# Performance work log

Measured on AMD Instinct MI355X. Metric: run time of the kernel, lower is better.

## Reference

```python
import jax, jax.numpy as jnp
from jax import lax
import numpy as np

K = 4            # prototypes per class: 3 kmeans centroids + 1 backbone
EPS = 0.1        # sinkhorn entropic regularization
MAX_ITER = 100
THRESH = 0.01
KM_ITERS = 10    # Lloyd iterations (replaces host-side sklearn KMeans)
HW = 28          # the original reshapes pred to 28x28, fixing n = 784


def setup_inputs():
    key = jax.random.key(0)
    k1, k2, k3, k4 = jax.random.split(key, 4)
    b, n, d, c = 32, HW * HW, 1024, 20
    return {
        "query": jax.random.normal(k1, (b, n, d), dtype=jnp.float32),
        "score": jax.random.uniform(k2, (b, n, c), dtype=jnp.float32),
        "label": jax.random.randint(k3, (b, c), 0, 2),
        "gt": jax.random.randint(k4, (b, HW, HW), 0, c + 1),
        "weights": jnp.array([1.0, 1.0, 0.0, -1.0], dtype=jnp.float32),
    }


def _assign(dq, cen, selfm):
    # dq [b,m,d], cen [b,c,j,d], selfm [b,c,m] float mask -> one-hot labels, counts
    x2 = jnp.sum(dq * dq, axis=-1)                                   # [b,m]
    d2 = (x2[:, None, :, None]
          - 2.0 * jnp.einsum('bmd,bcjd->bcmj', dq, cen)
          + jnp.sum(cen * cen, axis=-1)[:, :, None, :])              # [b,c,m,j]
    oh = jax.nn.one_hot(jnp.argmin(d2, axis=-1), cen.shape[2], dtype=dq.dtype) * selfm[..., None]
    return oh, oh.sum(axis=2)


def _sinkhorn(Km, u, v):
    # vectorized over the [b,c] pair grid, per-pair early exit as in the torch loop
    def cond(st):
        it, r, cc, done = st
        return (it < MAX_ITER) & jnp.logical_not(jnp.all(done))

    def body(st):
        it, r, cc, done = st
        r1 = u / jnp.einsum('bcnj,bcj->bcn', Km, cc)
        c1 = v / jnp.einsum('bcnj,bcn->bcj', Km, r1)
        err = jnp.mean(jnp.abs(r1 - r), axis=-1)                     # [b,c]
        r = jnp.where(done[..., None], r, r1)
        cc = jnp.where(done[..., None], cc, c1)
        done = done | (err < THRESH)
        return it + 1, r, cc, done

    st = (jnp.int32(0), jnp.ones_like(u), jnp.ones_like(v),
          jnp.zeros(Km.shape[:2], dtype=bool))
    _, r, cc, _ = lax.while_loop(cond, body, st)
    return r[..., :, None] * cc[..., None, :] * Km                   # [b,c,n,K]


def _forward(query, score, label, gt, weights):
    b, n, d = query.shape
    c = score.shape[2]
    dq, ds = query[:, ::2, :], score[:, ::2, :]                      # stride-2 downsample
    m = dq.shape[1]
    cls_assign = jnp.argmax(ds, axis=-1)                             # [b,m]
    sel = cls_assign[:, None, :] == jnp.arange(c)[None, :, None]     # [b,c,m]
    selfm = sel.astype(query.dtype)
    cnt = selfm.sum(-1)                                              # [b,c]
    valid = (label > 0) & (cnt >= K)

    # ---- masked Lloyd's k-means with k-1 = 3 clusters per (image, class) pair
    order = jnp.argsort((~sel).astype(jnp.int32), axis=-1)           # masked points first
    init_idx = order[..., :K - 1]                                    # [b,c,3]
    cen = dq[jnp.arange(b)[:, None, None], init_idx]                 # [b,c,3,d]

    def km_step(cen, _):
        oh, kcnt = _assign(dq, cen, selfm)
        sums = jnp.einsum('bmd,bcmj->bcjd', dq, oh)
        cen = jnp.where(kcnt[..., None] > 0,
                        sums / jnp.maximum(kcnt, 1.0)[..., None], cen)
        return cen, None

    cen, _ = lax.scan(km_step, cen, None, length=KM_ITERS)
    oh, kcnt = _assign(dq, cen, selfm)                               # final labels

    # ---- sort centroids by mean cluster score (descending)
    sm = ds.mean(axis=-1)                                            # [b,m]
    avg = jnp.where(kcnt > 0,
                    jnp.einsum('bm,bcmj->bcj', sm, oh) / jnp.maximum(kcnt, 1.0),
                    -jnp.inf)
    ordj = jnp.argsort(-avg, axis=-1)                                # [b,c,3]
    cen = jnp.take_along_axis(cen, ordj[..., None], axis=2)

    # ---- backbone prototype = mean over unselected downsampled tokens
    un = 1.0 - selfm
    backbone = jnp.einsum('bmd,bcm->bcd', dq, un) / jnp.maximum(m - cnt, 1.0)[..., None]
    protos = jnp.concatenate([cen, backbone[:, :, None, :]], axis=2)  # [b,c,4,d]

    # ---- OT between query[0] tokens and the 4 prototypes (original uses query[0] always)
    q0 = query[0]
    q0h = q0 / jnp.maximum(jnp.linalg.norm(q0, axis=-1, keepdims=True), 1e-12)
    ph = protos / jnp.maximum(jnp.linalg.norm(protos, axis=-1, keepdims=True), 1e-12)
    sim = jnp.einsum('nd,bcjd->bcnj', q0h, ph)                       # [b,c,n,4]
    Km = lax.stop_gradient(jnp.exp(-(1.0 - sim) / EPS))              # torch.no_grad
    u = jnp.full((b, c, n), 1.0 / n, dtype=query.dtype)
    v = jnp.full((b, c, K), 1.0 / K, dtype=query.dtype)
    T = lax.stop_gradient(_sinkhorn(Km, u, v))                       # [b,c,n,4]

    valid = valid & jnp.logical_not(jnp.any(jnp.isnan(T), axis=(2, 3)))
    pred = jnp.einsum('bcnj,j->bcn', T, weights)                     # [b,c,n]

    # ---- BCE vs gt masks (28x28 -> 28x28 bilinear resize is the identity)
    y = (gt.reshape(b, -1)[:, None, :] == (jnp.arange(c) + 1)[None, :, None]).astype(pred.dtype)
    p = jnp.clip(pred, 0.0, 1.0)
    bce = -(y * jnp.maximum(jnp.log(p), -100.0)
            + (1.0 - y) * jnp.maximum(jnp.log(1.0 - p), -100.0)).mean(axis=-1)  # [b,c]
    bce = jnp.where(valid, bce, 0.0)
    total_n = valid.sum().astype(pred.dtype)
    return bce.sum() / (total_n + 1e-4)


def reference(query, score, label, gt, weights):
    return _forward(query, score, label, gt, weights)
```

## Files before the change

kernel.cpp:

```cpp
#include <hip/hip_runtime.h>
#include <cmath>

#define BB 32
#define NN 784
#define MM 392
#define DD 1024
#define CC 20
#define JJ 3
#define KP 4
#define KM_ITERS 10
#define GMAX 64
#define SKK 3

__global__ void k_cls(const float* __restrict__ score, int* __restrict__ cls,
                      float* __restrict__ sm, int* __restrict__ cnt) {
  int t = blockIdx.x * blockDim.x + threadIdx.x;
  if (t >= BB * MM) return;
  int b = t / MM, i = t - b * MM;
  const float* s = score + ((size_t)b * NN + 2 * i) * CC;
  float best = s[0]; int bi = 0; float acc = s[0];
  #pragma unroll
  for (int c = 1; c < CC; c++) { float v = s[c]; acc += v; if (v > best) { best = v; bi = c; } }
  cls[t] = bi;
  sm[t] = acc / (float)CC;
  atomicAdd(&cnt[b * CC + bi], 1);
}

__global__ void k_valid(const int* __restrict__ label, const int* __restrict__ cnt,
                        int* __restrict__ vlist, int* __restrict__ cpos, int* __restrict__ nvp) {
  __shared__ int sf[1024];
  int t = threadIdx.x;
  int flag = 0;
  if (t < BB * CC) flag = (label[t] > 0 && cnt[t] >= KP) ? 1 : 0;
  sf[t] = flag;
  __syncthreads();
  for (int off = 1; off < 1024; off <<= 1) {
    int v = sf[t];
    int add = (t >= off) ? sf[t - off] : 0;
    __syncthreads();
    sf[t] = v + add;
    __syncthreads();
  }
  if (t < BB * CC) {
    int pos = sf[t] - flag;
    cpos[t] = flag ? pos : -1;
    if (flag) vlist[pos] = t;
  }
  if (t == 0) *nvp = sf[BB * CC - 1];
}

__global__ __launch_bounds__(512) void k_gram(
    const float* __restrict__ query, const int* __restrict__ cls,
    const int* __restrict__ cpos, const float* __restrict__ sm,
    float* __restrict__ classsum, float* __restrict__ ph) {
  int bc = blockIdx.x; int b = bc / CC, c = bc - b * CC;
  int tid = threadIdx.x, lane = tid & 63, wv = tid >> 6;
  const float* qb = query + (size_t)b * NN * DD;
  __shared__ int s_scan[512];
  __shared__ int s_list[GMAX];
  __shared__ __align__(16) float Xs[GMAX][68];
  __shared__ float Gl[GMAX][65];
  __shared__ float s_w[JJ][GMAX];
  __shared__ int s_rank[JJ];

  int flag = 0;
  if (tid < MM) flag = (cls[b * MM + tid] == c) ? 1 : 0;
  s_scan[tid] = flag;
  __syncthreads();
  for (int off = 1; off < 512; off <<= 1) {
    int v = s_scan[tid];
    int add = (tid >= off) ? s_scan[tid - off] : 0;
    __syncthreads();
    s_scan[tid] = v + add;
    __syncthreads();
  }
  if (tid < MM && flag) { int pp = s_scan[tid] - 1; if (pp < GMAX) s_list[pp] = tid; }
  __syncthreads();
  int mc = s_scan[MM - 1]; if (mc > GMAX) mc = GMAX;
  bool valid = (cpos[bc] >= 0);

  const float* pbase0 = nullptr; const float* pbase1 = nullptr;
  float* xdst0 = nullptr; float* xdst1 = nullptr;
  {
    int e0 = tid;
    if (e0 < mc * 16) {
      pbase0 = qb + (size_t)(2 * s_list[e0 >> 4]) * DD + (e0 & 15) * 4;
      xdst0 = &Xs[e0 >> 4][(e0 & 15) * 4];
    }
    int e1 = tid + 512;
    if (e1 < mc * 16) {
      pbase1 = qb + (size_t)(2 * s_list[e1 >> 4]) * DD + (e1 & 15) * 4;
      xdst1 = &Xs[e1 >> 4][(e1 & 15) * 4];
    }
  }

  int npairs = mc * (mc + 1) / 2;
  int pi[5], pj[5];
  float pacc[5];
  #pragma unroll
  for (int s = 0; s < 5; s++) {
    pacc[s] = 0.f; pi[s] = -1; pj[s] = 0;
    int p = tid + s * 512;
    if (valid && p < npairs) {
      int i = (int)floorf((sqrtf(8.0f * (float)p + 1.0f) - 1.0f) * 0.5f);
      while ((i + 1) * (i + 2) / 2 <= p) i++;
      while (i * (i + 1) / 2 > p) i--;
      pi[s] = i; pj[s] = p - i * (i + 1) / 2;
    }
  }

  float4 cur0, cur1, nxt0, nxt1;
  if (pbase0) cur0 = *(const float4*)(pbase0);
  if (pbase1) cur1 = *(const float4*)(pbase1);
  for (int ch = 0; ch < 16; ch++) {
    __syncthreads();
    if (pbase0) *(float4*)xdst0 = cur0;
    if (pbase1) *(float4*)xdst1 = cur1;
    if (ch < 15) {
      if (pbase0) nxt0 = *(const float4*)(pbase0 + (ch + 1) * 64);
      if (pbase1) nxt1 = *(const float4*)(pbase1 + (ch + 1) * 64);
    }
    __syncthreads();
    #pragma unroll
    for (int s = 0; s < 5; s++) {
      if (pi[s] >= 0) {
        const float4* xi = (const float4*)&Xs[pi[s]][0];
        const float4* xj = (const float4*)&Xs[pj[s]][0];
        float a = 0.f;
        #pragma unroll
        for (int kk = 0; kk < 16; kk++) {
          float4 u = xi[kk], w = xj[kk];
          a += u.x * w.x + u.y * w.y + u.z * w.z + u.w * w.w;
        }
        pacc[s] += a;
      }
    }
    if (tid >= 448) {
      int col = tid - 448;
      float ssum = 0.f;
      for (int row = 0; row < mc; row++) ssum += Xs[row][col];
      classsum[(size_t)bc * DD + ch * 64 + col] = ssum;
    }
    cur0 = nxt0; cur1 = nxt1;
  }
  if (!valid) return;

  #pragma unroll
  for (int s = 0; s < 5; s++)
    if (pi[s] >= 0) { Gl[pi[s]][pj[s]] = pacc[s]; Gl[pj[s]][pi[s]] = pacc[s]; }
  __syncthreads();

  if (wv == 0) {
    bool act = lane < mc;
    float smv = act ? sm[b * MM + s_list[lane]] : 0.f;
    s_w[0][lane] = (lane == 0) ? 1.f : 0.f;
    s_w[1][lane] = (lane == 1) ? 1.f : 0.f;
    s_w[2][lane] = (lane == 2) ? 1.f : 0.f;
    int aj = 0, n0 = 0, n1 = 0, n2 = 0;
    for (int it = 0; it <= KM_ITERS; it++) {
      float h0 = 0.f, h1 = 0.f, h2 = 0.f;
      if (act) {
        for (int i = 0; i < mc; i++) {
          float g = Gl[lane][i];
          h0 += s_w[0][i] * g; h1 += s_w[1][i] * g; h2 += s_w[2][i] * g;
        }
      }
      float t0 = s_w[0][lane] * h0, t1 = s_w[1][lane] * h1, t2 = s_w[2][lane] * h2;
      for (int o = 1; o < 64; o <<= 1) {
        t0 += __shfl_xor(t0, o, 64); t1 += __shfl_xor(t1, o, 64); t2 += __shfl_xor(t2, o, 64);
      }
      float e0 = t0 - 2.f * h0, e1 = t1 - 2.f * h1, e2 = t2 - 2.f * h2;
      aj = 0; float bv = e0;
      if (e1 < bv) { bv = e1; aj = 1; }
      if (e2 < bv) { bv = e2; aj = 2; }
      n0 = __popcll(__ballot(act && aj == 0));
      n1 = __popcll(__ballot(act && aj == 1));
      n2 = __popcll(__ballot(act && aj == 2));
      if (it == KM_ITERS) break;
      if (act) {
        if (n0 > 0) s_w[0][lane] = (aj == 0) ? 1.f / (float)n0 : 0.f;
        if (n1 > 0) s_w[1][lane] = (aj == 1) ? 1.f / (float)n1 : 0.f;
        if (n2 > 0) s_w[2][lane] = (aj == 2) ? 1.f / (float)n2 : 0.f;
      }
    }
    float s0 = (act && aj == 0) ? smv : 0.f;
    float s1 = (act && aj == 1) ? smv : 0.f;
    float s2 = (act && aj == 2) ? smv : 0.f;
    for (int o = 1; o < 64; o <<= 1) {
      s0 += __shfl_xor(s0, o, 64); s1 += __shfl_xor(s1, o, 64); s2 += __shfl_xor(s2, o, 64);
    }
    if (lane == 0) {
      float avg[JJ];
      avg[0] = (n0 > 0) ? s0 / (float)n0 : -INFINITY;
      avg[1] = (n1 > 0) ? s1 / (float)n1 : -INFINITY;
      avg[2] = (n2 > 0) ? s2 / (float)n2 : -INFINITY;
      bool used[JJ] = {false, false, false};
      for (int s = 0; s < JJ; s++) {
        int bi = -1; float bv = 0.f;
        for (int j = 0; j < JJ; j++)
          if (!used[j] && (bi < 0 || avg[j] > bv)) { bi = j; bv = avg[j]; }
        used[bi] = true; s_rank[bi] = s;
      }
    }
  }
  __syncthreads();

  float cenv[16];
  if (pbase0) cur0 = *(const float4*)(pbase0);
  if (pbase1) cur1 = *(const float4*)(pbase1);
  for (int ch = 0; ch < 16; ch++) {
    __syncthreads();
    if (pbase0) *(float4*)xdst0 = cur0;
    if (pbase1) *(float4*)xdst1 = cur1;
    if (ch < 15) {
      if (pbase0) nxt0 = *(const float4*)(pbase0 + (ch + 1) * 64);
      if (pbase1) nxt1 = *(const float4*)(pbase1 + (ch + 1) * 64);
    }
    __syncthreads();
    if (tid < 192) {
      int j = tid >> 6, l = tid & 63;
      float a = 0.f;
      for (int g = 0; g < mc; g++) a += s_w[j][g] * Xs[g][l];
      cenv[ch] = a;
    }
    cur0 = nxt0; cur1 = nxt1;
  }
  if (tid < 192) {
    int j = tid >> 6, l = tid & 63;
    float ssq = 0.f;
    #pragma unroll
    for (int ch = 0; ch < 16; ch++) ssq += cenv[ch] * cenv[ch];
    for (int o = 1; o < 64; o <<= 1) ssq += __shfl_xor(ssq, o, 64);
    float nrm = fmaxf(sqrtf(ssq), 1e-12f);
    float* dst = ph + ((size_t)bc * KP + s_rank[j]) * DD + l;
    #pragma unroll
    for (int ch = 0; ch < 16; ch++) dst[ch * 64] = cenv[ch] / nrm;
  }
}

__global__ __launch_bounds__(256) void k_backbone(const float* __restrict__ classsum,
    const int* __restrict__ cpos, const int* __restrict__ cnt, float* __restrict__ ph) {
  int bc = blockIdx.x;
  if (cpos[bc] < 0) return;
  int b = bc / CC;
  int tid = threadIdx.x, lane = tid & 63, wv = tid >> 6;
  __shared__ float s_red[4];
  __shared__ float s_nrm;
  float4 ts = make_float4(0.f, 0.f, 0.f, 0.f);
  for (int c2 = 0; c2 < CC; c2++) {
    float4 v = *(const float4*)(classsum + ((size_t)(b * CC + c2)) * DD + tid * 4);
    ts.x += v.x; ts.y += v.y; ts.z += v.z; ts.w += v.w;
  }
  float4 cs = *(const float4*)(classsum + (size_t)bc * DD + tid * 4);
  float denom = fmaxf((float)(MM - cnt[bc]), 1.f);
  float4 v = make_float4((ts.x - cs.x) / denom, (ts.y - cs.y) / denom,
                         (ts.z - cs.z) / denom, (ts.w - cs.w) / denom);
  float pp = v.x * v.x + v.y * v.y + v.z * v.z + v.w * v.w;
  for (int o = 1; o < 64; o <<= 1) pp += __shfl_xor(pp, o, 64);
  if (lane == 0) s_red[wv] = pp;
  __syncthreads();
  if (tid == 0) s_nrm = fmaxf(sqrtf(s_red[0] + s_red[1] + s_red[2] + s_red[3]), 1e-12f);
  __syncthreads();
  float nrm = s_nrm;
  *(float4*)(ph + ((size_t)bc * KP + 3) * DD + tid * 4) =
      make_float4(v.x / nrm, v.y / nrm, v.z / nrm, v.w / nrm);
}

__global__ void k_q0h(const float* __restrict__ query, float* __restrict__ q0h) {
  int n = blockIdx.x;
  const float* src = query + (size_t)n * DD;
  float ss = 0.f;
  for (int k = threadIdx.x; k < DD; k += 64) { float v = src[k]; ss += v * v; }
  for (int o = 32; o > 0; o >>= 1) ss += __shfl_xor(ss, o, 64);
  float nrm = fmaxf(sqrtf(ss), 1e-12f);
  for (int k = threadIdx.x; k < DD; k += 64) q0h[(size_t)n * DD + k] = src[k] / nrm;
}

__global__ __launch_bounds__(256) void k_gemm(const float* __restrict__ A,
    const float* __restrict__ ph, const int* __restrict__ vlist,
    const int* __restrict__ nvp, float* __restrict__ P) {
  int nv4 = 4 * *nvp;
  int n0 = blockIdx.y * 64;
  if (n0 >= nv4) return;
  __shared__ float As[64][20];
  __shared__ float Bs[64][20];
  int tx = threadIdx.x & 15, ty = threadIdx.x >> 4;
  int m0 = blockIdx.x * 64;
  int s = blockIdx.z;
  int lrow = threadIdx.x >> 2;
  int lk = (threadIdx.x & 3) * 4;
  int brow = n0 + lrow;
  bool bval = brow < nv4;
  const float* Brow = ph;
  if (bval) {
    int bcc = brow >> 2;
    Brow = ph + ((size_t)vlist[bcc] * KP + (brow & 3)) * DD;
  }
  float acc[4][4] = {};
  int kbase = s * 352;
  int kend = (kbase + 352 < DD) ? (kbase + 352) : DD;
  for (int k0 = kbase; k0 < kend; k0 += 16) {
    int ar = m0 + lrow;
    float4 av = (ar < NN) ? *(const float4*)(A + (size_t)ar * DD + k0 + lk)
                          : make_float4(0.f, 0.f, 0.f, 0.f);
    *(float4*)&As[lrow][lk] = av;
    float4 bv = bval ? *(const float4*)(Brow + k0 + lk)
                     : make_float4(0.f, 0.f, 0.f, 0.f);
    *(float4*)&Bs[lrow][lk] = bv;
    __syncthreads();
    #pragma unroll
    for (int kk = 0; kk < 16; kk += 4) {
      float4 a4[4], b4[4];
      #pragma unroll
      for (int i = 0; i < 4; i++) a4[i] = *(const float4*)&As[ty * 4 + i][kk];
      #pragma unroll
      for (int j = 0; j < 4; j++) b4[j] = *(const float4*)&Bs[tx + 16 * j][kk];
      #pragma unroll
      for (int i = 0; i < 4; i++)
        #pragma unroll
        for (int j = 0; j < 4; j++) {
          acc[i][j] += a4[i].x * b4[j].x;
          acc[i][j] += a4[i].y * b4[j].y;
          acc[i][j] += a4[i].z * b4[j].z;
          acc[i][j] += a4[i].w * b4[j].w;
        }
    }
    __syncthreads();
  }
  #pragma unroll
  for (int i = 0; i < 4; i++) {
    int mr = m0 + ty * 4 + i;
    if (mr >= NN) continue;
    float* row = P + ((size_t)s * NN + mr) * (size_t)(BB * CC * KP) + n0 + tx;
    #pragma unroll
    for (int j = 0; j < 4; j++) row[16 * j] = acc[i][j];
  }
}

__global__ __launch_bounds__(256) void k_sink(const float* __restrict__ P,
    const int* __restrict__ cpos, const int* __restrict__ gt,
    const float* __restrict__ wts, float* __restrict__ bce, int* __restrict__ vld) {
  int bc = blockIdx.x; int b = bc / CC, c = bc - b * CC;
  int tid = threadIdx.x;
  if (cpos[bc] < 0) {
    if (tid == 0) { bce[bc] = 0.f; vld[bc] = 0; }
    return;
  }
  int p = cpos[bc];
  int lane = tid & 63, wv = tid >> 6;
  __shared__ float ccv[KP];
  __shared__ float wred[4][5];
  __shared__ float s_err;
  __shared__ int s_nan;
  const float4* P4 = (const float4*)P;
  float4 kv[4]; float rr[4];
  #pragma unroll
  for (int s = 0; s < 4; s++) {
    int n = tid + 256 * s;
    kv[s] = make_float4(0.f, 0.f, 0.f, 0.f); rr[s] = 1.f;
    if (n < NN) {
      float4 a = P4[(size_t)(0 * NN + n) * (BB * CC) + p];
      float4 b2 = P4[(size_t)(1 * NN + n) * (BB * CC) + p];
      float4 c2 = P4[(size_t)(2 * NN + n) * (BB * CC) + p];
      float4 o;
      o.x = expf(-(1.0f - (a.x + b2.x + c2.x)) / 0.1f);
      o.y = expf(-(1.0f - (a.y + b2.y + c2.y)) / 0.1f);
      o.z = expf(-(1.0f - (a.z + b2.z + c2.z)) / 0.1f);
      o.w = expf(-(1.0f - (a.w + b2.w + c2.w)) / 0.1f);
      kv[s] = o;
    }
  }
  if (tid < KP) ccv[tid] = 1.f;
  if (tid == 0) s_nan = 0;
  __syncthreads();
  const float uu = 1.0f / (float)NN, vv = 1.0f / (float)KP;
  for (int it = 0; it < 100; it++) {
    float c0 = ccv[0], c1 = ccv[1], c2 = ccv[2], c3 = ccv[3];
    float dsum = 0.f, p0 = 0.f, p1 = 0.f, p2 = 0.f, p3 = 0.f;
    #pragma unroll
    for (int s = 0; s < 4; s++) {
      int n = tid + 256 * s;
      if (n < NN) {
        float4 k4 = kv[s];
        float S = k4.x * c0 + k4.y * c1 + k4.z * c2 + k4.w * c3;
        float r1 = uu / S;
        dsum += fabsf(r1 - rr[s]);
        rr[s] = r1;
        p0 += k4.x * r1; p1 += k4.y * r1; p2 += k4.z * r1; p3 += k4.w * r1;
      }
    }
    for (int o = 32; o > 0; o >>= 1) {
      dsum += __shfl_down(dsum, o, 64);
      p0 += __shfl_down(p0, o, 64); p1 += __shfl_down(p1, o, 64);
      p2 += __shfl_down(p2, o, 64); p3 += __shfl_down(p3, o, 64);
    }
    if (lane == 0) { wred[wv][0] = dsum; wred[wv][1] = p0; wred[wv][2] = p1; wred[wv][3] = p2; wred[wv][4] = p3; }
    __syncthreads();
    if (tid == 0) {
      float d = 0.f, q0 = 0.f, q1 = 0.f, q2 = 0.f, q3 = 0.f;
      for (int w = 0; w < 4; w++) { d += wred[w][0]; q0 += wred[w][1]; q1 += wred[w][2]; q2 += wred[w][3]; q3 += wred[w][4]; }
      ccv[0] = vv / q0; ccv[1] = vv / q1; ccv[2] = vv / q2; ccv[3] = vv / q3;
      s_err = d / (float)NN;
    }
    __syncthreads();
    if (s_err < 0.01f) break;
  }
  float w0 = wts[0], w1 = wts[1], w2 = wts[2], w3 = wts[3];
  float cc0 = ccv[0], cc1 = ccv[1], cc2 = ccv[2], cc3 = ccv[3];
  float bsum = 0.f; int nanloc = 0;
  const int* gtb = gt + b * NN;
  #pragma unroll
  for (int s = 0; s < 4; s++) {
    int n = tid + 256 * s;
    if (n < NN) {
      float4 k4 = kv[s];
      float rv = rr[s];
      float T0 = rv * cc0 * k4.x, T1 = rv * cc1 * k4.y, T2 = rv * cc2 * k4.z, T3 = rv * cc3 * k4.w;
      if (T0 != T0 || T1 != T1 || T2 != T2 || T3 != T3) nanloc = 1;
      float pred = T0 * w0 + T1 * w1 + T2 * w2 + T3 * w3;
      float pcl = fminf(fmaxf(pred, 0.f), 1.f);
      float t = (gtb[n] == c + 1) ? fmaxf(logf(pcl), -100.f) : fmaxf(logf(1.f - pcl), -100.f);
      bsum += t;
    }
  }
  if (nanloc) s_nan = 1;
  for (int o = 32; o > 0; o >>= 1) bsum += __shfl_down(bsum, o, 64);
  if (lane == 0) wred[wv][0] = bsum;
  __syncthreads();
  if (tid == 0) {
    float tot = wred[0][0] + wred[1][0] + wred[2][0] + wred[3][0];
    if (s_nan) { bce[bc] = 0.f; vld[bc] = 0; }
    else { bce[bc] = -(tot / (float)NN); vld[bc] = 1; }
  }
}

__global__ void k_final(const float* __restrict__ bce, const int* __restrict__ vld,
                        float* __restrict__ out) {
  __shared__ float rs[256];
  __shared__ float rc[256];
  float s = 0.f, cv = 0.f;
  for (int t = threadIdx.x; t < BB * CC; t += 256) { s += bce[t]; cv += (float)vld[t]; }
  rs[threadIdx.x] = s; rc[threadIdx.x] = cv; __syncthreads();
  for (int o = 128; o > 0; o >>= 1) {
    if (threadIdx.x < o) { rs[threadIdx.x] += rs[threadIdx.x + o]; rc[threadIdx.x] += rc[threadIdx.x + o]; }
    __syncthreads();
  }
  if (threadIdx.x == 0) out[0] = rs[0] / (rc[0] + 0.0001f);
}

extern "C" void kernel_launch(void* const* d_in, const int* in_sizes, int n_in,
                              void* d_out, int out_size, void* d_ws, size_t ws_size,
                              hipStream_t stream) {
  (void)in_sizes; (void)n_in; (void)out_size; (void)ws_size;
  const float* query = (const float*)d_in[0];
  const float* score = (const float*)d_in[1];
  const int*   label = (const int*)d_in[2];
  const int*   gt    = (const int*)d_in[3];
  const float* wts   = (const float*)d_in[4];
  float* ws = (float*)d_ws;

  size_t off = 0;
  int* cls = (int*)(ws + off);       off += (size_t)BB * MM;
  int* cnt = (int*)(ws + off);       off += (size_t)BB * CC;
  float* sm = ws + off;              off += (size_t)BB * MM;
  int* vlist = (int*)(ws + off);     off += (size_t)BB * CC;
  int* cpos = (int*)(ws + off);      off += (size_t)BB * CC;
  int* nvp = (int*)(ws + off);       off += 16;
  float* classsum = ws + off;        off += (size_t)BB * CC * DD;
  float* ph = ws + off;              off += (size_t)BB * CC * KP * DD;
  float* q0h = ws + off;             off += (size_t)NN * DD;
  float* P = ws + off;               off += (size_t)SKK * NN * BB * CC * KP;
  float* bce = ws + off;             off += (size_t)BB * CC;
  int* vld = (int*)(ws + off);       off += (size_t)BB * CC;

  hipMemsetAsync(cnt, 0, (size_t)BB * CC * sizeof(int), stream);
  k_cls<<<(BB * MM + 255) / 256, 256, 0, stream>>>(score, cls, sm, cnt);
  k_valid<<<1, 1024, 0, stream>>>(label, cnt, vlist, cpos, nvp);
  k_gram<<<BB * CC, 512, 0, stream>>>(query, cls, cpos, sm, classsum, ph);
  k_backbone<<<BB * CC, 256, 0, stream>>>(classsum, cpos, cnt, ph);
  k_q0h<<<NN, 64, 0, stream>>>(query, q0h);
  dim3 gg((NN + 63) / 64, (BB * CC * KP) / 64, SKK);
  k_gemm<<<gg, 256, 0, stream>>>(q0h, ph, vlist, nvp, P);
  k_sink<<<BB * CC, 256, 0, stream>>>(P, cpos, gt, wts, bce, vld);
  k_final<<<1, 256, 0, stream>>>(bce, vld, (float*)d_out);
}
```

Measured before the change: 294.4 us.

## Register-tile Gram computation and transpose partial-GEMM output layout for sinkhorn reads

The Gram kernel now has 136 threads each compute a 4x4 tile of the upper-triangle of the 64x64 Gram matrix. This replaces the per-pair dot products with their repeated shared-memory reads and the sqrt-based index decode. Separately, the split-K GEMM now writes its partial results column-major (column, then n), so each sinkhorn block reads contiguous n-strided data for its four prototype columns instead of float4 gathers strided by the full column count. The GEMM stores become strided per thread, trading write coalescing for read coalescing in the sinkhorn.

Result: slower. 511.8 us (+73.8%).

```diff
diff --git a/kernel.cpp b/kernel.cpp
--- a/kernel.cpp
+++ b/kernel.cpp
@@ -11,6 +11,7 @@
 #define KM_ITERS 10
 #define GMAX 64
 #define SKK 3
+#define NCOL (BB * CC * KP)
 
 __global__ void k_cls(const float* __restrict__ score, int* __restrict__ cls,
                       float* __restrict__ sm, int* __restrict__ cnt) {
@@ -94,20 +95,21 @@
     }
   }
 
-  int npairs = mc * (mc + 1) / 2;
-  int pi[5], pj[5];
-  float pacc[5];
+  int ti = -1, tj = 0;
+  if (valid && tid < 136) {
+    int t = tid;
+    for (int r = 0; r < 16; r++) {
+      int w = 16 - r;
+      if (t < w) { ti = r; tj = r + t; break; }
+      t -= w;
+    }
+  }
+  bool work = (ti >= 0) && (4 * ti < mc) && (4 * tj < mc);
+  float acc[4][4];
   #pragma unroll
-  for (int s = 0; s < 5; s++) {
-    pacc[s] = 0.f; pi[s] = -1; pj[s] = 0;
-    int p = tid + s * 512;
-    if (valid && p < npairs) {
-      int i = (int)floorf((sqrtf(8.0f * (float)p + 1.0f) - 1.0f) * 0.5f);
-      while ((i + 1) * (i + 2) / 2 <= p) i++;
-      while (i * (i + 1) / 2 > p) i--;
-      pi[s] = i; pj[s] = p - i * (i + 1) / 2;
-    }
-  }
+  for (int i = 0; i < 4; i++)
+    #pragma unroll
+    for (int j = 0; j < 4; j++) acc[i][j] = 0.f;
 
   float4 cur0, cur1, nxt0, nxt1;
   if (pbase0) cur0 = *(const float4*)(pbase0);
@@ -121,18 +123,20 @@
       if (pbase1) nxt1 = *(const float4*)(pbase1 + (ch + 1) * 64);
     }
     __syncthreads();
-    #pragma unroll
-    for (int s = 0; s < 5; s++) {
-      if (pi[s] >= 0) {
-        const float4* xi = (const float4*)&Xs[pi[s]][0];
-        const float4* xj = (const float4*)&Xs[pj[s]][0];
-        float a = 0.f;
+    if (work) {
+      #pragma unroll
+      for (int kkg = 0; kkg < 16; kkg++) {
+        float4 a4[4], b4[4];
         #pragma unroll
-        for (int kk = 0; kk < 16; kk++) {
-          float4 u = xi[kk], w = xj[kk];
-          a += u.x * w.x + u.y * w.y + u.z * w.z + u.w * w.w;
-        }
-        pacc[s] += a;
+        for (int i = 0; i < 4; i++) a4[i] = *(const float4*)&Xs[4 * ti + i][kkg * 4];
+        #pragma unroll
+        for (int j = 0; j < 4; j++) b4[j] = *(const float4*)&Xs[4 * tj + j][kkg * 4];
+        #pragma unroll
+        for (int i = 0; i < 4; i++)
+          #pragma unroll
+          for (int j = 0; j < 4; j++)
+            acc[i][j] += a4[i].x * b4[j].x + a4[i].y * b4[j].y +
+                         a4[i].z * b4[j].z + a4[i].w * b4[j].w;
       }
     }
     if (tid >= 448) {
@@ -145,9 +149,15 @@
   }
   if (!valid) return;
 
-  #pragma unroll
-  for (int s = 0; s < 5; s++)
-    if (pi[s] >= 0) { Gl[pi[s]][pj[s]] = pacc[s]; Gl[pj[s]][pi[s]] = pacc[s]; }
+  if (work) {
+    #pragma unroll
+    for (int i = 0; i < 4; i++)
+      #pragma unroll
+      for (int j = 0; j < 4; j++) {
+        Gl[4 * ti + i][4 * tj + j] = acc[i][j];
+        Gl[4 * tj + j][4 * ti + i] = acc[i][j];
+      }
+  }
   __syncthreads();
 
   if (wv == 0) {
@@ -328,12 +338,14 @@
     __syncthreads();
   }
   #pragma unroll
-  for (int i = 0; i < 4; i++) {
-    int mr = m0 + ty * 4 + i;
-    if (mr >= NN) continue;
-    float* row = P + ((size_t)s * NN + mr) * (size_t)(BB * CC * KP) + n0 + tx;
-    #pragma unroll
-    for (int j = 0; j < 4; j++) row[16 * j] = acc[i][j];
+  for (int j = 0; j < 4; j++) {
+    int col = n0 + tx + 16 * j;
+    float* cb = P + ((size_t)s * NCOL + col) * NN + m0 + ty * 4;
+    #pragma unroll
+    for (int i = 0; i < 4; i++) {
+      int mr = m0 + ty * 4 + i;
+      if (mr < NN) cb[i] = acc[i][j];
+    }
   }
 }
 
@@ -352,22 +364,24 @@
   __shared__ float wred[4][5];
   __shared__ float s_err;
   __shared__ int s_nan;
-  const float4* P4 = (const float4*)P;
   float4 kv[4]; float rr[4];
   #pragma unroll
-  for (int s = 0; s < 4; s++) {
-    int n = tid + 256 * s;
-    kv[s] = make_float4(0.f, 0.f, 0.f, 0.f); rr[s] = 1.f;
+  for (int s4 = 0; s4 < 4; s4++) {
+    int n = tid + 256 * s4;
+    kv[s4] = make_float4(0.f, 0.f, 0.f, 0.f); rr[s4] = 1.f;
     if (n < NN) {
-      float4 a = P4[(size_t)(0 * NN + n) * (BB * CC) + p];
-      float4 b2 = P4[(size_t)(1 * NN + n) * (BB * CC) + p];
-      float4 c2 = P4[(size_t)(2 * NN + n) * (BB * CC) + p];
+      float v[KP] = {0.f, 0.f, 0.f, 0.f};
+      #pragma unroll
+      for (int s = 0; s < SKK; s++)
+        #pragma unroll
+        for (int q = 0; q < KP; q++)
+          v[q] += P[((size_t)s * NCOL + 4 * p + q) * NN + n];
       float4 o;
-      o.x = expf(-(1.0f - (a.x + b2.x + c2.x)) / 0.1f);
-      o.y = expf(-(1.0f - (a.y + b2.y + c2.y)) / 0.1f);
-      o.z = expf(-(1.0f - (a.z + b2.z + c2.z)) / 0.1f);
-      o.w = expf(-(1.0f - (a.w + b2.w + c2.w)) / 0.1f);
-      kv[s] = o;
+      o.x = expf(-(1.0f - v[0]) / 0.1f);
+      o.y = expf(-(1.0f - v[1]) / 0.1f);
+      o.z = expf(-(1.0f - v[2]) / 0.1f);
+      o.w = expf(-(1.0f - v[3]) / 0.1f);
+      kv[s4] = o;
     }
   }
   if (tid < KP) ccv[tid] = 1.f;
@@ -378,14 +392,14 @@
     float c0 = ccv[0], c1 = ccv[1], c2 = ccv[2], c3 = ccv[3];
     float dsum = 0.f, p0 = 0.f, p1 = 0.f, p2 = 0.f, p3 = 0.f;
     #pragma unroll
-    for (int s = 0; s < 4; s++) {
-      int n = tid + 256 * s;
+    for (int s4 = 0; s4 < 4; s4++) {
+      int n = tid + 256 * s4;
       if (n < NN) {
-        float4 k4 = kv[s];
+        float4 k4 = kv[s4];
         float S = k4.x * c0 + k4.y * c1 + k4.z * c2 + k4.w * c3;
         float r1 = uu / S;
-        dsum += fabsf(r1 - rr[s]);
-        rr[s] = r1;
+        dsum += fabsf(r1 - rr[s4]);
+        rr[s4] = r1;
         p0 += k4.x * r1; p1 += k4.y * r1; p2 += k4.z * r1; p3 += k4.w * r1;
       }
     }
@@ -410,11 +424,11 @@
   float bsum = 0.f; int nanloc = 0;
   const int* gtb = gt + b * NN;
   #pragma unroll
-  for (int s = 0; s < 4; s++) {
-    int n = tid + 256 * s;
+  for (int s4 = 0; s4 < 4; s4++) {
+    int n = tid + 256 * s4;
     if (n < NN) {
-      float4 k4 = kv[s];
-      float rv = rr[s];
+      float4 k4 = kv[s4];
+      float rv = rr[s4];
       float T0 = rv * cc0 * k4.x, T1 = rv * cc1 * k4.y, T2 = rv * cc2 * k4.z, T3 = rv * cc3 * k4.w;
       if (T0 != T0 || T1 != T1 || T2 != T2 || T3 != T3) nanloc = 1;
       float pred = T0 * w0 + T1 * w1 + T2 * w2 + T3 * w3;
@@ -469,7 +483,7 @@
   float* classsum = ws + off;        off += (size_t)BB * CC * DD;
   float* ph = ws + off;              off += (size_t)BB * CC * KP * DD;
   float* q0h = ws + off;             off += (size_t)NN * DD;
-  float* P = ws + off;               off += (size_t)SKK * NN * BB * CC * KP;
+  float* P = ws + off;               off += (size_t)SKK * NN * NCOL;
   float* bce = ws + off;             off += (size_t)BB * CC;
   int* vld = (int*)(ws + off);       off += (size_t)BB * CC;
 
```
